# Kernel optimization log

Hardware: AMD Instinct MI355X
Metric: run time of the kernel (lower is better)

Reference implementation:

```python
import jax, jax.numpy as jnp
import numpy as np

B, C, HF, WF = 4, 64, 48, 48      # LR feature map
HQ, WQ = 384, 384                 # HR query grid
OUT, HID = 3, 256                 # imnet out_dim / hidden width
IN_DIM = C + 4 + 3                # q_feat + rel_coord(2) + rel_cell(2) + rgb_std(3)


def _grid_sample_nearest(img, gx, gy):
    # PyTorch grid_sample(mode='nearest', align_corners=False, padding_mode='zeros')
    Hin, Win = img.shape[-2], img.shape[-1]
    ix = ((gx + 1.0) * Win - 1.0) * 0.5
    iy = ((gy + 1.0) * Hin - 1.0) * 0.5
    ixn = jnp.round(ix).astype(jnp.int32)   # round-half-even matches nearbyint
    iyn = jnp.round(iy).astype(jnp.int32)
    valid = (ixn >= 0) & (ixn < Win) & (iyn >= 0) & (iyn < Hin)
    ixc = jnp.clip(ixn, 0, Win - 1)
    iyc = jnp.clip(iyn, 0, Hin - 1)
    out = jax.vmap(lambda im, yy, xx: im[:, yy, xx])(img, iyc, ixc)  # [B,C,Hq,Wq]
    return jnp.where(valid[:, None], out, jnp.zeros((), out.dtype))


def _make_feat_coord(h, w, dtype):
    # LIIF make_coord: pixel-center coords in [-1, 1], (y, x) order -> [2, h, w]
    ys = (2.0 * jnp.arange(h, dtype=dtype) + 1.0) / h - 1.0
    xs = (2.0 * jnp.arange(w, dtype=dtype) + 1.0) / w - 1.0
    yy, xx = jnp.meshgrid(ys, xs, indexing='ij')
    return jnp.stack([yy, xx], axis=0)


def setup_inputs() -> dict:
    key = jax.random.key(0)
    ks = jax.random.split(key, 16)
    x = jax.random.normal(ks[0], (B, C, HF, WF), dtype=jnp.float32)
    coord = jax.random.uniform(ks[1], (B, HQ, WQ, 2), dtype=jnp.float32,
                               minval=-1.0, maxval=1.0)
    cell = jnp.broadcast_to(jnp.array([2.0 / HQ, 2.0 / WQ], jnp.float32)[None, :],
                            (B, 2)).copy()
    lr = jax.random.normal(ks[2], (B, 3, HF, WF), dtype=jnp.float32)
    dims = [IN_DIM, HID, HID, HID, HID, OUT]
    params = {}
    for i in range(5):
        fi, fo = dims[i], dims[i + 1]
        params[f'W{i}'] = jax.random.normal(ks[3 + i], (fi, fo), jnp.float32) / np.sqrt(fi)
        params[f'b{i}'] = jax.random.normal(ks[8 + i], (fo,), jnp.float32) * 0.01
    return {'x': x, 'coord': coord, 'cell': cell, 'lr': lr, **params}


def _forward(x, coord, cell, lr, W0, b0, W1, b1, W2, b2, W3, b3, W4, b4):
    b, c, hf, wf = x.shape
    feat_coord = jnp.broadcast_to(_make_feat_coord(hf, wf, x.dtype)[None],
                                  (b, 2, hf, wf))
    gy = coord[..., 0]
    gx = coord[..., 1]  # coord.flip(-1): grid_sample takes (x, y)
    q_feat = _grid_sample_nearest(x, gx, gy)            # [B,C,HQ,WQ]
    q_coord = _grid_sample_nearest(feat_coord, gx, gy)  # [B,2,HQ,WQ]
    scale = jnp.array([hf, wf], x.dtype).reshape(1, 2, 1, 1)
    rel_coord = (jnp.transpose(coord, (0, 3, 1, 2)) - q_coord) * scale
    rel_cell = (cell * jnp.array([hf, wf], x.dtype))[:, :, None, None]
    rel_cell = jnp.broadcast_to(rel_cell, (b, 2, coord.shape[1], coord.shape[2]))
    inp = jnp.concatenate([q_feat, rel_coord, rel_cell], axis=1)

    # add_type == 1: std over 4 diagonally shifted nearest LR samples
    rx = 1.0 / hf
    ry = 1.0 / wf
    eps = 1e-6
    lo, hi = -1.0 + 1e-6, 1.0 - 1e-6
    q_rgbs = []
    for vx in (-1.0, 1.0):
        for vy in (-1.0, 1.0):
            cy = jnp.clip(gy + vx * rx + eps, lo, hi)
            cx = jnp.clip(gx + vy * ry + eps, lo, hi)
            q_rgbs.append(_grid_sample_nearest(lr, cx, cy))
    rgb_std = jnp.std(jnp.stack(q_rgbs, axis=0), axis=0, ddof=1)  # unbiased (torch.std)
    inp = jnp.concatenate([inp, rgb_std], axis=1)  # [B, C+7, HQ, WQ]

    # imnet(inp.transpose(1,3)).transpose(1,3)
    h = jnp.transpose(inp, (0, 3, 2, 1))  # [B, WQ, HQ, C+7]
    for Wm, bm in ((W0, b0), (W1, b1), (W2, b2), (W3, b3)):
        h = jax.nn.relu(h @ Wm + bm)
    h = h @ W4 + b4                       # [B, WQ, HQ, OUT]
    return jnp.transpose(h, (0, 3, 2, 1))  # [B, OUT, HQ, WQ]


def reference(x, coord, cell, lr, W0, b0, W1, b1, W2, b2, W3, b3, W4, b4):
    return _forward(x, coord, cell, lr, W0, b0, W1, b1, W2, b2, W3, b3, W4, b4)
```

## Files before the change

kernel.cpp:

```cpp
#include <hip/hip_runtime.h>

#pragma clang fp contract(off)

#define HQ 384
#define WQ 384
#define NC 64
#define HFD 48
#define HID 256
#define NPIX (4 * HQ * WQ)
#define PPB 128
#define NTHR 512

typedef _Float16 half8 __attribute__((ext_vector_type(8)));
typedef __fp16 fp16x2 __attribute__((ext_vector_type(2)));
typedef float f32x4 __attribute__((ext_vector_type(4)));
typedef unsigned int u32;
typedef unsigned short u16;

#define O0H 0
#define O0L 12288
#define O1H 24576
#define O1L 57344
#define O2H 90112
#define O2L 122880
#define O3H 155648
#define O3L 188416
#define O4H 221184
#define O4L 223232

__device__ __forceinline__ u32 pkrtz(float a, float b) {
    fp16x2 h = __builtin_amdgcn_cvt_pkrtz(a, b);
    return __builtin_bit_cast(u32, h);
}

__device__ __forceinline__ int nearest_idx(float g, bool& valid) {
    float t  = (g + 1.0f) * 48.0f;
    float ix = (t - 1.0f) * 0.5f;
    float r  = rintf(ix);
    int   i  = (int)r;
    if (i < 0 || i > 47) valid = false;
    return i < 0 ? 0 : (i > 47 ? 47 : i);
}

extern "C" __global__ void __launch_bounds__(256)
pack_w(const float* __restrict__ W0, const float* __restrict__ W1,
       const float* __restrict__ W2, const float* __restrict__ W3,
       const float* __restrict__ W4, u32* __restrict__ ws) {
    int gid = blockIdx.x * 256 + threadIdx.x;
    const float* W; int NS, K, oh, ol, rem; bool isW4 = false;
    if (gid < 12288)       { W = W0; NS = 3; K = 71;  oh = O0H; ol = O0L; rem = gid; }
    else if (gid < 45056)  { W = W1; NS = 8; K = 256; oh = O1H; ol = O1L; rem = gid - 12288; }
    else if (gid < 77824)  { W = W2; NS = 8; K = 256; oh = O2H; ol = O2L; rem = gid - 45056; }
    else if (gid < 110592) { W = W3; NS = 8; K = 256; oh = O3H; ol = O3L; rem = gid - 77824; }
    else                   { W = W4; NS = 8; K = 256; oh = O4H; ol = O4L; rem = gid - 110592; isW4 = true; }
    int i = rem & 3, lane = (rem >> 2) & 63, ts = rem >> 8;
    int s = ts % NS, t = ts / NS;
    int jp = t * 16 + (lane & 15);
    int k0 = s * 32 + (lane >> 4) * 8 + 2 * i;
    float w0, w1;
    if (isW4) {
        w0 = (jp < 3 && k0 < K)     ? W[(size_t)k0 * 3 + jp]       : 0.0f;
        w1 = (jp < 3 && k0 + 1 < K) ? W[(size_t)(k0 + 1) * 3 + jp] : 0.0f;
    } else {
        w0 = (k0 < K)     ? W[(size_t)k0 * HID + jp]       : 0.0f;
        w1 = (k0 + 1 < K) ? W[(size_t)(k0 + 1) * HID + jp] : 0.0f;
    }
    _Float16 h0 = (_Float16)w0, h1 = (_Float16)w1;
    _Float16 l0 = (_Float16)(w0 - (float)h0);
    _Float16 l1 = (_Float16)(w1 - (float)h1);
    ws[oh + rem] = (u32)__builtin_bit_cast(u16, h0) | ((u32)__builtin_bit_cast(u16, h1) << 16);
    ws[ol + rem] = (u32)__builtin_bit_cast(u16, l0) | ((u32)__builtin_bit_cast(u16, l1) << 16);
}

template <int NS, bool USELO>
__device__ __forceinline__ void mfma_layer(
    const u32* __restrict__ whi, const u32* __restrict__ wlo,
    const float* __restrict__ bias,
    u32* __restrict__ sAct, int wave, int lane) {
    const int r = lane & 15, g = lane >> 4;
    const int ph = wave >> 2;
    const int wj = wave & 3;
    f32x4 acc[4][4];
#pragma unroll
    for (int a = 0; a < 4; ++a)
#pragma unroll
        for (int b = 0; b < 4; ++b) acc[a][b] = f32x4{0.0f, 0.0f, 0.0f, 0.0f};

    auto sstep = [&](int s) {
        half8 ah[4], al[4];
#pragma unroll
        for (int tt = 0; tt < 4; ++tt) {
            int idx = (((wj * 4 + tt) * NS + s) * 64 + lane) * 4;
            ah[tt] = __builtin_bit_cast(half8, *(const uint4*)(whi + idx));
            if constexpr (USELO)
                al[tt] = __builtin_bit_cast(half8, *(const uint4*)(wlo + idx));
        }
#pragma unroll
        for (int p = 0; p < 4; ++p) {
            int rr = ph * 64 + p * 16 + r;
            int u = (s * 4 + g) ^ (rr & 31);
            half8 bh = __builtin_bit_cast(half8, *(const uint4*)(sAct + rr * 128 + u * 4));
#pragma unroll
            for (int tt = 0; tt < 4; ++tt) {
                if constexpr (USELO)
                    acc[tt][p] = __builtin_amdgcn_mfma_f32_16x16x32_f16(al[tt], bh, acc[tt][p], 0, 0, 0);
                acc[tt][p] = __builtin_amdgcn_mfma_f32_16x16x32_f16(ah[tt], bh, acc[tt][p], 0, 0, 0);
            }
        }
    };
    if constexpr (USELO) {
#pragma unroll 1
        for (int s = 0; s < NS; ++s) sstep(s);
    } else {
#pragma unroll 2
        for (int s = 0; s < NS; ++s) sstep(s);
    }
    __syncthreads();

#pragma unroll
    for (int tt = 0; tt < 4; ++tt) {
        int T = wj * 4 + tt;
        int jb = T * 16 + g * 4;
        float bv0 = bias[jb + 0], bv1 = bias[jb + 1];
        float bv2 = bias[jb + 2], bv3 = bias[jb + 3];
#pragma unroll
        for (int p = 0; p < 4; ++p) {
            float v0 = fmaxf(acc[tt][p][0] + bv0, 0.0f);
            float v1 = fmaxf(acc[tt][p][1] + bv1, 0.0f);
            float v2 = fmaxf(acc[tt][p][2] + bv2, 0.0f);
            float v3 = fmaxf(acc[tt][p][3] + bv3, 0.0f);
            int rr = ph * 64 + p * 16 + r;
            int u = (2 * T + (g >> 1)) ^ (rr & 31);
            int a = rr * 128 + u * 4 + (g & 1) * 2;
            sAct[a]     = pkrtz(v0, v1);
            sAct[a + 1] = pkrtz(v2, v3);
        }
    }
    __syncthreads();
}

extern "C" __global__ void __launch_bounds__(NTHR, 4)
liif_mfma(const float* __restrict__ x, const float* __restrict__ coord,
          const float* __restrict__ cell, const float* __restrict__ lr,
          const float* __restrict__ b0, const float* __restrict__ b1,
          const float* __restrict__ b2, const float* __restrict__ b3,
          const float* __restrict__ b4,
          const u32* __restrict__ ws, float* __restrict__ out) {
    __shared__ u32 sAct[PPB * 128];
    const int tid = threadIdx.x;
    const int wave = tid >> 6, lane = tid & 63;

    {
        const int px = tid >> 2, sub = tid & 3;
        const int gg = blockIdx.x * PPB + px;
        const int b = gg / (HQ * WQ);
        const float gy = coord[(size_t)gg * 2 + 0];
        const float gx = coord[(size_t)gg * 2 + 1];
        bool vmain = true;
        const int ixn = nearest_idx(gx, vmain);
        const int iyn = nearest_idx(gy, vmain);

        const float* xb = x + (((size_t)b * NC) * HFD + iyn) * HFD + ixn;
        u32 hbuf[8];
#pragma unroll
        for (int e = 0; e < 8; ++e) {
            int c = sub * 16 + e * 2;
            float v0 = vmain ? xb[(size_t)c * (HFD * HFD)] : 0.0f;
            float v1 = vmain ? xb[(size_t)(c + 1) * (HFD * HFD)] : 0.0f;
            hbuf[e] = pkrtz(v0, v1);
        }
        {
            int u = (2 * sub) ^ (px & 31);
            *(uint4*)(sAct + px * 128 + u * 4) = make_uint4(hbuf[0], hbuf[1], hbuf[2], hbuf[3]);
            u = (2 * sub + 1) ^ (px & 31);
            *(uint4*)(sAct + px * 128 + u * 4) = make_uint4(hbuf[4], hbuf[5], hbuf[6], hbuf[7]);
        }
        if (sub == 0) {
            float qyc = vmain ? ((2.0f * (float)iyn + 1.0f) / 48.0f - 1.0f) : 0.0f;
            float qxc = vmain ? ((2.0f * (float)ixn + 1.0f) / 48.0f - 1.0f) : 0.0f;
            float f64v = (gy - qyc) * 48.0f;
            float f65v = (gx - qxc) * 48.0f;
            float f66v = cell[b * 2 + 0] * 48.0f;
            float f67v = cell[b * 2 + 1] * 48.0f;

            const float c148 = (float)(1.0 / 48.0);
            const float LO = (float)(-1.0 + 1e-6);
            const float HI = (float)(1.0 - 1e-6);
            float v[4][3];
#pragma unroll
            for (int a = 0; a < 2; ++a) {
                const float vx = (a == 0) ? -c148 : c148;
#pragma unroll
                for (int qq = 0; qq < 2; ++qq) {
                    const float vy = (qq == 0) ? -c148 : c148;
                    float cy = (gy + vx) + 1e-6f;
                    cy = fminf(fmaxf(cy, LO), HI);
                    float cx = (gx + vy) + 1e-6f;
                    cx = fminf(fmaxf(cx, LO), HI);
                    bool vv = true;
                    int jx = nearest_idx(cx, vv);
                    int jy = nearest_idx(cy, vv);
                    int si = a * 2 + qq;
#pragma unroll
                    for (int ch = 0; ch < 3; ++ch)
                        v[si][ch] = vv ? lr[(((size_t)b * 3 + ch) * HFD + jy) * HFD + jx] : 0.0f;
                }
            }
            float sd[3];
#pragma unroll
            for (int ch = 0; ch < 3; ++ch) {
                float mean = (((v[0][ch] + v[1][ch]) + v[2][ch]) + v[3][ch]) / 4.0f;
                float d0 = v[0][ch] - mean, d1 = v[1][ch] - mean;
                float d2 = v[2][ch] - mean, d3 = v[3][ch] - mean;
                float var = (((d0 * d0 + d1 * d1) + d2 * d2) + d3 * d3) / 3.0f;
                sd[ch] = sqrtf(var);
            }
            int u = 8 ^ (px & 31);
            *(uint4*)(sAct + px * 128 + u * 4) =
                make_uint4(pkrtz(f64v, f65v), pkrtz(f66v, f67v),
                           pkrtz(sd[0], sd[1]), pkrtz(sd[2], 0.0f));
        } else {
            int u = (8 + sub) ^ (px & 31);
            *(uint4*)(sAct + px * 128 + u * 4) = make_uint4(0, 0, 0, 0);
        }
    }
    __syncthreads();

    mfma_layer<3, true >(ws + O0H, ws + O0L, b0, sAct, wave, lane);
    mfma_layer<8, false>(ws + O1H, ws + O1L, b1, sAct, wave, lane);
    mfma_layer<8, false>(ws + O2H, ws + O2L, b2, sAct, wave, lane);
    mfma_layer<8, false>(ws + O3H, ws + O3L, b3, sAct, wave, lane);

    {
        const int r = lane & 15, g = lane >> 4;
        const int rr = wave * 16 + r;
        f32x4 acc = f32x4{0.0f, 0.0f, 0.0f, 0.0f};
#pragma unroll
        for (int s = 0; s < 8; ++s) {
            int idx = (s * 64 + lane) * 4;
            half8 ah = __builtin_bit_cast(half8, *(const uint4*)(ws + O4H + idx));
            half8 al = __builtin_bit_cast(half8, *(const uint4*)(ws + O4L + idx));
            int u = (s * 4 + g) ^ (rr & 31);
            half8 bh = __builtin_bit_cast(half8, *(const uint4*)(sAct + rr * 128 + u * 4));
            acc = __builtin_amdgcn_mfma_f32_16x16x32_f16(al, bh, acc, 0, 0, 0);
            acc = __builtin_amdgcn_mfma_f32_16x16x32_f16(ah, bh, acc, 0, 0, 0);
        }
        if (g == 0) {
            int px = wave * 16 + r;
            int gg = blockIdx.x * PPB + px;
            int b = gg / (HQ * WQ);
            int rem = gg - b * (HQ * WQ);
#pragma unroll
            for (int o = 0; o < 3; ++o)
                out[((size_t)(b * 3 + o)) * (HQ * WQ) + rem] = acc[o] + b4[o];
        }
    }
}

extern "C" void kernel_launch(void* const* d_in, const int* in_sizes, int n_in,
                              void* d_out, int out_size, void* d_ws, size_t ws_size,
                              hipStream_t stream) {
    const float* x     = (const float*)d_in[0];
    const float* coord = (const float*)d_in[1];
    const float* cell  = (const float*)d_in[2];
    const float* lr    = (const float*)d_in[3];
    const float* W0    = (const float*)d_in[4];
    const float* b0    = (const float*)d_in[5];
    const float* W1    = (const float*)d_in[6];
    const float* b1    = (const float*)d_in[7];
    const float* W2    = (const float*)d_in[8];
    const float* b2    = (const float*)d_in[9];
    const float* W3    = (const float*)d_in[10];
    const float* b3    = (const float*)d_in[11];
    const float* W4    = (const float*)d_in[12];
    const float* b4    = (const float*)d_in[13];
    u32* ws = (u32*)d_ws;

    pack_w<<<dim3(440), dim3(256), 0, stream>>>(W0, W1, W2, W3, W4, ws);
    liif_mfma<<<dim3(NPIX / PPB), dim3(NTHR), 0, stream>>>(
        x, coord, cell, lr, b0, b1, b2, b3, b4, ws, (float*)d_out);
}
```

Baseline: 418.8 us.

## Switch hidden MLP layers from 16x16x32 to 32x32x16 MFMA tiles

Replaces the 16x16x32 MFMA tiling (each wave computing 64 output columns by 64 pixels) with 32x32x16 MFMA instructions, where each wave owns 32 output columns across all 128 pixels. The weight pre-packing kernel is rewritten to match the new K-step and column layout. Each wave now loads one weight fragment per k-step instead of four, which cuts global weight traffic and register pressure, while reading four times as many activation fragments from LDS. The larger MFMA shape may also give higher throughput per instruction.

```diff
diff --git a/kernel.cpp b/kernel.cpp
--- a/kernel.cpp
+++ b/kernel.cpp
@@ -14,6 +14,7 @@
 typedef _Float16 half8 __attribute__((ext_vector_type(8)));
 typedef __fp16 fp16x2 __attribute__((ext_vector_type(2)));
 typedef float f32x4 __attribute__((ext_vector_type(4)));
+typedef float f32x16 __attribute__((ext_vector_type(16)));
 typedef unsigned int u32;
 typedef unsigned short u16;
 
@@ -48,20 +49,22 @@
        const float* __restrict__ W4, u32* __restrict__ ws) {
     int gid = blockIdx.x * 256 + threadIdx.x;
     const float* W; int NS, K, oh, ol, rem; bool isW4 = false;
-    if (gid < 12288)       { W = W0; NS = 3; K = 71;  oh = O0H; ol = O0L; rem = gid; }
-    else if (gid < 45056)  { W = W1; NS = 8; K = 256; oh = O1H; ol = O1L; rem = gid - 12288; }
-    else if (gid < 77824)  { W = W2; NS = 8; K = 256; oh = O2H; ol = O2L; rem = gid - 45056; }
-    else if (gid < 110592) { W = W3; NS = 8; K = 256; oh = O3H; ol = O3L; rem = gid - 77824; }
-    else                   { W = W4; NS = 8; K = 256; oh = O4H; ol = O4L; rem = gid - 110592; isW4 = true; }
+    if (gid < 12288)       { W = W0; NS = 6;  K = 71;  oh = O0H; ol = O0L; rem = gid; }
+    else if (gid < 45056)  { W = W1; NS = 16; K = 256; oh = O1H; ol = O1L; rem = gid - 12288; }
+    else if (gid < 77824)  { W = W2; NS = 16; K = 256; oh = O2H; ol = O2L; rem = gid - 45056; }
+    else if (gid < 110592) { W = W3; NS = 16; K = 256; oh = O3H; ol = O3L; rem = gid - 77824; }
+    else                   { W = W4; NS = 8;  K = 256; oh = O4H; ol = O4L; rem = gid - 110592; isW4 = true; }
     int i = rem & 3, lane = (rem >> 2) & 63, ts = rem >> 8;
     int s = ts % NS, t = ts / NS;
-    int jp = t * 16 + (lane & 15);
-    int k0 = s * 32 + (lane >> 4) * 8 + 2 * i;
     float w0, w1;
     if (isW4) {
+        int jp = lane & 15;
+        int k0 = s * 32 + (lane >> 4) * 8 + 2 * i;
         w0 = (jp < 3 && k0 < K)     ? W[(size_t)k0 * 3 + jp]       : 0.0f;
         w1 = (jp < 3 && k0 + 1 < K) ? W[(size_t)(k0 + 1) * 3 + jp] : 0.0f;
     } else {
+        int jp = t * 32 + (lane & 31);
+        int k0 = s * 16 + (lane >> 5) * 8 + 2 * i;
         w0 = (k0 < K)     ? W[(size_t)k0 * HID + jp]       : 0.0f;
         w1 = (k0 + 1 < K) ? W[(size_t)(k0 + 1) * HID + jp] : 0.0f;
     }
@@ -73,65 +76,49 @@
 }
 
 template <int NS, bool USELO>
-__device__ __forceinline__ void mfma_layer(
+__device__ __forceinline__ void mfma_layer32(
     const u32* __restrict__ whi, const u32* __restrict__ wlo,
     const float* __restrict__ bias,
     u32* __restrict__ sAct, int wave, int lane) {
-    const int r = lane & 15, g = lane >> 4;
-    const int ph = wave >> 2;
-    const int wj = wave & 3;
-    f32x4 acc[4][4];
-#pragma unroll
-    for (int a = 0; a < 4; ++a)
-#pragma unroll
-        for (int b = 0; b < 4; ++b) acc[a][b] = f32x4{0.0f, 0.0f, 0.0f, 0.0f};
-
-    auto sstep = [&](int s) {
-        half8 ah[4], al[4];
-#pragma unroll
-        for (int tt = 0; tt < 4; ++tt) {
-            int idx = (((wj * 4 + tt) * NS + s) * 64 + lane) * 4;
-            ah[tt] = __builtin_bit_cast(half8, *(const uint4*)(whi + idx));
+    const int col = lane & 31, hi = lane >> 5;
+    f32x16 acc[4];
+#pragma unroll
+    for (int p = 0; p < 4; ++p)
+#pragma unroll
+        for (int e = 0; e < 16; ++e) acc[p][e] = 0.0f;
+
+#pragma unroll 2
+    for (int s = 0; s < NS; ++s) {
+        int idx = ((wave * NS + s) * 64 + lane) * 4;
+        half8 ah = __builtin_bit_cast(half8, *(const uint4*)(whi + idx));
+        half8 al;
+        if constexpr (USELO)
+            al = __builtin_bit_cast(half8, *(const uint4*)(wlo + idx));
+#pragma unroll
+        for (int p = 0; p < 4; ++p) {
+            int rr = p * 32 + col;
+            int u = (s * 2 + hi) ^ (rr & 31);
+            half8 bh = __builtin_bit_cast(half8, *(const uint4*)(sAct + rr * 128 + u * 4));
             if constexpr (USELO)
-                al[tt] = __builtin_bit_cast(half8, *(const uint4*)(wlo + idx));
-        }
+                acc[p] = __builtin_amdgcn_mfma_f32_32x32x16_f16(al, bh, acc[p], 0, 0, 0);
+            acc[p] = __builtin_amdgcn_mfma_f32_32x32x16_f16(ah, bh, acc[p], 0, 0, 0);
+        }
+    }
+    __syncthreads();
+
+#pragma unroll
+    for (int grp = 0; grp < 4; ++grp) {
+        int jb = wave * 32 + hi * 4 + grp * 8;
+        float4 bv = *(const float4*)(bias + jb);
 #pragma unroll
         for (int p = 0; p < 4; ++p) {
-            int rr = ph * 64 + p * 16 + r;
-            int u = (s * 4 + g) ^ (rr & 31);
-            half8 bh = __builtin_bit_cast(half8, *(const uint4*)(sAct + rr * 128 + u * 4));
-#pragma unroll
-            for (int tt = 0; tt < 4; ++tt) {
-                if constexpr (USELO)
-                    acc[tt][p] = __builtin_amdgcn_mfma_f32_16x16x32_f16(al[tt], bh, acc[tt][p], 0, 0, 0);
-                acc[tt][p] = __builtin_amdgcn_mfma_f32_16x16x32_f16(ah[tt], bh, acc[tt][p], 0, 0, 0);
-            }
-        }
-    };
-    if constexpr (USELO) {
-#pragma unroll 1
-        for (int s = 0; s < NS; ++s) sstep(s);
-    } else {
-#pragma unroll 2
-        for (int s = 0; s < NS; ++s) sstep(s);
-    }
-    __syncthreads();
-
-#pragma unroll
-    for (int tt = 0; tt < 4; ++tt) {
-        int T = wj * 4 + tt;
-        int jb = T * 16 + g * 4;
-        float bv0 = bias[jb + 0], bv1 = bias[jb + 1];
-        float bv2 = bias[jb + 2], bv3 = bias[jb + 3];
-#pragma unroll
-        for (int p = 0; p < 4; ++p) {
-            float v0 = fmaxf(acc[tt][p][0] + bv0, 0.0f);
-            float v1 = fmaxf(acc[tt][p][1] + bv1, 0.0f);
-            float v2 = fmaxf(acc[tt][p][2] + bv2, 0.0f);
-            float v3 = fmaxf(acc[tt][p][3] + bv3, 0.0f);
-            int rr = ph * 64 + p * 16 + r;
-            int u = (2 * T + (g >> 1)) ^ (rr & 31);
-            int a = rr * 128 + u * 4 + (g & 1) * 2;
+            float v0 = fmaxf(acc[p][grp * 4 + 0] + bv.x, 0.0f);
+            float v1 = fmaxf(acc[p][grp * 4 + 1] + bv.y, 0.0f);
+            float v2 = fmaxf(acc[p][grp * 4 + 2] + bv.z, 0.0f);
+            float v3 = fmaxf(acc[p][grp * 4 + 3] + bv.w, 0.0f);
+            int rr = p * 32 + col;
+            int u = (wave * 4 + grp) ^ (rr & 31);
+            int a = rr * 128 + u * 4 + hi * 2;
             sAct[a]     = pkrtz(v0, v1);
             sAct[a + 1] = pkrtz(v2, v3);
         }
@@ -226,10 +213,10 @@
     }
     __syncthreads();
 
-    mfma_layer<3, true >(ws + O0H, ws + O0L, b0, sAct, wave, lane);
-    mfma_layer<8, false>(ws + O1H, ws + O1L, b1, sAct, wave, lane);
-    mfma_layer<8, false>(ws + O2H, ws + O2L, b2, sAct, wave, lane);
-    mfma_layer<8, false>(ws + O3H, ws + O3L, b3, sAct, wave, lane);
+    mfma_layer32<6,  true >(ws + O0H, ws + O0L, b0, sAct, wave, lane);
+    mfma_layer32<16, false>(ws + O1H, ws + O1L, b1, sAct, wave, lane);
+    mfma_layer32<16, false>(ws + O2H, ws + O2L, b2, sAct, wave, lane);
+    mfma_layer32<16, false>(ws + O3H, ws + O3L, b3, sAct, wave, lane);
 
     {
         const int r = lane & 15, g = lane >> 4;
```

Result: slower. 449.2 us (+7.3%).
